# Kernel tuning notes

Measured on AMD Instinct MI355X. Metric: run time of the kernel, lower is better.

The kernel has to match this reference:

```python
import jax, jax.numpy as jnp
import numpy as np
from jax import lax

BIG = 1e10  # initial 'infinite' distance, matching torch's 1e10


def farthest_point_sample(xyz, npoint):
    # xyz: [B, N, 3] float; returns centroids: [B, npoint] int32
    B, N, _ = xyz.shape

    def step(carry, _):
        distance, farthest = carry            # [B,N], [B]
        # gather current farthest point per batch -> [B,1,3]
        centroid = jnp.take_along_axis(xyz, farthest[:, None, None], axis=1)
        dist = jnp.sum((xyz - centroid) ** 2, axis=-1)   # [B,N]
        distance = jnp.minimum(distance, dist)           # running min distance
        new_farthest = jnp.argmax(distance, axis=-1).astype(jnp.int32)
        # emit the index selected at THIS iteration (torch stores before update)
        return (distance, new_farthest), farthest

    init = (jnp.full((B, N), BIG, dtype=xyz.dtype),
            jnp.zeros((B,), dtype=jnp.int32))
    _, centroids = lax.scan(step, init, None, length=npoint)  # [npoint, B]
    return centroids.T  # [B, npoint]


def setup_inputs() -> dict:
    key = jax.random.key(0)
    B, N = 8, 131072
    xyz = jax.random.normal(key, (B, N, 3), dtype=jnp.float32)
    return {"xyz": xyz, "points": 1024}


def reference(xyz, points):
    return farthest_point_sample(xyz, points)
```

## Files before the change

kernel.cpp:

```cpp
#include <hip/hip_runtime.h>
#include <stdint.h>


#define NPTS        131072
#define NBATCH      8
#define WGB         32
#define THREADS     256
#define PPW         4096
#define SLOT_STRIDE 16
#define BIGDIST     1e10f

__global__ __launch_bounds__(THREADS, 1) void fps_kernel(
        const float* __restrict__ xyz,
        int* __restrict__ out,
        unsigned long long* __restrict__ slots,
        int npoint)
{
    const int bid  = blockIdx.x;
    const int b    = bid & (NBATCH - 1);
    const int w    = bid >> 3;
    const int tid  = threadIdx.x;
    const int lane = tid & 63;
    const int wave = tid >> 6;

    const float* base = xyz + (size_t)b * NPTS * 3;
    const int q0 = w * PPW;

    __shared__ __align__(16) float x_lds[PPW];
    __shared__ __align__(16) float y_lds[PPW];
    __shared__ __align__(16) float z_lds[PPW];
    __shared__ unsigned long long s_w[THREADS / 64];
    __shared__ float s_c[3];

    #pragma unroll
    for (int j = 0; j < 16; ++j) {
        int q = tid + 256 * j;
        const float* p = base + (size_t)(q0 + q) * 3;
        x_lds[q] = p[0];
        y_lds[q] = p[1];
        z_lds[q] = p[2];
    }

    float dist[16];
    #pragma unroll
    for (int j = 0; j < 16; ++j) dist[j] = BIGDIST;

    float cx = base[0], cy = base[1], cz = base[2];

    if (w == 0 && tid == 0) out[b * npoint + 0] = 0;

    const size_t PAR = (size_t)NBATCH * WGB * SLOT_STRIDE;

    __syncthreads();

    for (int i = 0; i < npoint - 1; ++i) {
        float bv = -1.0f; int bq = 0;
        {
            #pragma clang fp contract(off)
            #pragma unroll
            for (int g = 0; g < 4; ++g) {
                const int qg = 4 * tid + 1024 * g;
                float4 xv = *reinterpret_cast<const float4*>(&x_lds[qg]);
                float4 yv = *reinterpret_cast<const float4*>(&y_lds[qg]);
                float4 zv = *reinterpret_cast<const float4*>(&z_lds[qg]);
                float xs[4] = { xv.x, xv.y, xv.z, xv.w };
                float ys[4] = { yv.x, yv.y, yv.z, yv.w };
                float zs[4] = { zv.x, zv.y, zv.z, zv.w };
                #pragma unroll
                for (int e = 0; e < 4; ++e) {
                    const int j = 4 * g + e;
                    float dx = xs[e] - cx, dy = ys[e] - cy, dz = zs[e] - cz;
                    float d  = dx*dx + dy*dy + dz*dz;
                    float nd = fminf(dist[j], d);
                    dist[j]  = nd;
                    if (nd > bv) { bv = nd; bq = qg + e; }
                }
            }
        }
        unsigned long long pk =
              ((unsigned long long)__float_as_uint(bv) << 32)
            | (unsigned long long)(0x1FFFFu - (unsigned)(q0 + bq));

        #pragma unroll
        for (int m = 32; m >= 1; m >>= 1) {
            unsigned long long o = __shfl_xor(pk, m);
            if (o > pk) pk = o;
        }
        if (lane == 0) s_w[wave] = pk;
        __syncthreads();

        unsigned long long* sb =
            slots + ((i & 1) ? PAR : (size_t)0) + (size_t)b * WGB * SLOT_STRIDE;
        const unsigned tag = (unsigned)(i + 1);

        if (wave == 0) {
            unsigned long long v = s_w[lane & 3];
            #pragma unroll
            for (int m = 2; m >= 1; m >>= 1) {
                unsigned long long o = __shfl_xor(v, m);
                if (o > v) v = o;
            }
            if (lane == 0) {
                unsigned long long pub = v | ((unsigned long long)tag << 22);
                __hip_atomic_store(sb + (size_t)w * SLOT_STRIDE, pub,
                                   __ATOMIC_RELAXED, __HIP_MEMORY_SCOPE_AGENT);
            }
            unsigned long long s = 0;
            if (lane < WGB) {
                unsigned long long* sl = sb + (size_t)lane * SLOT_STRIDE;
                do {
                    s = __hip_atomic_load(sl, __ATOMIC_RELAXED,
                                          __HIP_MEMORY_SCOPE_AGENT);
                } while (((unsigned)(s >> 22) & 1023u) != tag);
            }
            int idx_l = (int)(0x1FFFFu - (unsigned)(s & 0x1FFFFu));
            float ccx = 0.f, ccy = 0.f, ccz = 0.f;
            if (lane < WGB) {
                const float* cp = base + (size_t)idx_l * 3;
                ccx = cp[0]; ccy = cp[1]; ccz = cp[2];
            }
            unsigned long long mx = s;
            #pragma unroll
            for (int m = 16; m >= 1; m >>= 1) {
                unsigned long long o = __shfl_xor(mx, m);
                if (o > mx) mx = o;
            }
            unsigned long long ball = __ballot(lane < WGB && s == mx);
            int winlane = __ffsll(ball) - 1;
            float wx = __shfl(ccx, winlane);
            float wy = __shfl(ccy, winlane);
            float wz = __shfl(ccz, winlane);
            int  wix = __shfl(idx_l, winlane);
            if (lane == 0) {
                s_c[0] = wx; s_c[1] = wy; s_c[2] = wz;
                if (w == 0) out[b * npoint + (i + 1)] = wix;
            }
        }
        __syncthreads();

        cx = s_c[0]; cy = s_c[1]; cz = s_c[2];
    }
}

extern "C" void kernel_launch(void* const* d_in, const int* in_sizes, int n_in,
                              void* d_out, int out_size, void* d_ws, size_t ws_size,
                              hipStream_t stream) {
    const float* xyz = (const float*)d_in[0];
    int* out = (int*)d_out;
    unsigned long long* slots = (unsigned long long*)d_ws;
    const int npoint = out_size / NBATCH;

    hipMemsetAsync(d_ws, 0,
                   (size_t)2 * NBATCH * WGB * SLOT_STRIDE * sizeof(unsigned long long),
                   stream);

    dim3 grid(NBATCH * WGB);
    dim3 block(THREADS);
    fps_kernel<<<grid, block, 0, stream>>>(xyz, out, slots, npoint);
}
```

Baseline: 2.345 ms.

## Publish per-wave results globally and drop intra-block barriers in FPS loop

Each wave now publishes its own argmax candidate to a global slot (128 slots per batch instead of 32), and every wave independently polls all slots and reduces them. This removes both __syncthreads and the LDS hand-off of the centroid from every iteration. Point coordinates are also cached in registers instead of being reloaded from LDS each iteration. The trade-off is four times more global polling traffic and redundant reductions in every wave, plus higher register pressure.

```diff
diff --git a/kernel.cpp b/kernel.cpp
--- a/kernel.cpp
+++ b/kernel.cpp
@@ -7,6 +7,7 @@
 #define WGB         32
 #define THREADS     256
 #define PPW         4096
+#define NSLOT       (WGB * 4)
 #define SLOT_STRIDE 16
 #define BIGDIST     1e10f
 
@@ -21,7 +22,7 @@
     const int w    = bid >> 3;
     const int tid  = threadIdx.x;
     const int lane = tid & 63;
-    const int wave = tid >> 6;
+    const int v    = tid >> 6;
 
     const float* base = xyz + (size_t)b * NPTS * 3;
     const int q0 = w * PPW;
@@ -29,8 +30,6 @@
     __shared__ __align__(16) float x_lds[PPW];
     __shared__ __align__(16) float y_lds[PPW];
     __shared__ __align__(16) float z_lds[PPW];
-    __shared__ unsigned long long s_w[THREADS / 64];
-    __shared__ float s_c[3];
 
     #pragma unroll
     for (int j = 0; j < 16; ++j) {
@@ -40,7 +39,17 @@
         y_lds[q] = p[1];
         z_lds[q] = p[2];
     }
+    __syncthreads();
 
+    const int pbase = q0 + 1024 * v + 4 * lane;
+    float4 X[4], Y[4], Z[4];
+    #pragma unroll
+    for (int g = 0; g < 4; ++g) {
+        const int qg = 1024 * v + 4 * lane + 256 * g;
+        X[g] = *reinterpret_cast<const float4*>(&x_lds[qg]);
+        Y[g] = *reinterpret_cast<const float4*>(&y_lds[qg]);
+        Z[g] = *reinterpret_cast<const float4*>(&z_lds[qg]);
+    }
     float dist[16];
     #pragma unroll
     for (int j = 0; j < 16; ++j) dist[j] = BIGDIST;
@@ -49,23 +58,19 @@
 
     if (w == 0 && tid == 0) out[b * npoint + 0] = 0;
 
-    const size_t PAR = (size_t)NBATCH * WGB * SLOT_STRIDE;
-
-    __syncthreads();
+    const size_t PAR = (size_t)NBATCH * NSLOT * SLOT_STRIDE;
+    unsigned long long* sbase = slots + (size_t)b * NSLOT * SLOT_STRIDE;
+    const int sid = (w << 2) | v;
 
     for (int i = 0; i < npoint - 1; ++i) {
-        float bv = -1.0f; int bq = 0;
+        float bv = -1.0f; int boff = 0;
         {
             #pragma clang fp contract(off)
             #pragma unroll
             for (int g = 0; g < 4; ++g) {
-                const int qg = 4 * tid + 1024 * g;
-                float4 xv = *reinterpret_cast<const float4*>(&x_lds[qg]);
-                float4 yv = *reinterpret_cast<const float4*>(&y_lds[qg]);
-                float4 zv = *reinterpret_cast<const float4*>(&z_lds[qg]);
-                float xs[4] = { xv.x, xv.y, xv.z, xv.w };
-                float ys[4] = { yv.x, yv.y, yv.z, yv.w };
-                float zs[4] = { zv.x, zv.y, zv.z, zv.w };
+                float xs[4] = { X[g].x, X[g].y, X[g].z, X[g].w };
+                float ys[4] = { Y[g].x, Y[g].y, Y[g].z, Y[g].w };
+                float zs[4] = { Z[g].x, Z[g].y, Z[g].z, Z[g].w };
                 #pragma unroll
                 for (int e = 0; e < 4; ++e) {
                     const int j = 4 * g + e;
@@ -73,72 +78,63 @@
                     float d  = dx*dx + dy*dy + dz*dz;
                     float nd = fminf(dist[j], d);
                     dist[j]  = nd;
-                    if (nd > bv) { bv = nd; bq = qg + e; }
+                    if (nd > bv) { bv = nd; boff = 256 * g + e; }
                 }
             }
         }
         unsigned long long pk =
               ((unsigned long long)__float_as_uint(bv) << 32)
-            | (unsigned long long)(0x1FFFFu - (unsigned)(q0 + bq));
+            | (unsigned long long)(0x1FFFFu - (unsigned)(pbase + boff));
 
         #pragma unroll
         for (int m = 32; m >= 1; m >>= 1) {
             unsigned long long o = __shfl_xor(pk, m);
             if (o > pk) pk = o;
         }
-        if (lane == 0) s_w[wave] = pk;
-        __syncthreads();
 
-        unsigned long long* sb =
-            slots + ((i & 1) ? PAR : (size_t)0) + (size_t)b * WGB * SLOT_STRIDE;
+        unsigned long long* sb = sbase + ((i & 1) ? PAR : (size_t)0);
         const unsigned tag = (unsigned)(i + 1);
 
-        if (wave == 0) {
-            unsigned long long v = s_w[lane & 3];
-            #pragma unroll
-            for (int m = 2; m >= 1; m >>= 1) {
-                unsigned long long o = __shfl_xor(v, m);
-                if (o > v) v = o;
+        if (lane == 0) {
+            __hip_atomic_store(sb + (size_t)sid * SLOT_STRIDE,
+                               pk | ((unsigned long long)tag << 22),
+                               __ATOMIC_RELAXED, __HIP_MEMORY_SCOPE_AGENT);
+        }
+
+        unsigned long long* a0 = sb + (size_t)(2 * lane)     * SLOT_STRIDE;
+        unsigned long long* a1 = sb + (size_t)(2 * lane + 1) * SLOT_STRIDE;
+        unsigned long long s0 = 0, s1 = 0;
+        bool ok0 = false, ok1 = false;
+        do {
+            if (!ok0) {
+                s0 = __hip_atomic_load(a0, __ATOMIC_RELAXED, __HIP_MEMORY_SCOPE_AGENT);
+                ok0 = ((unsigned)(s0 >> 22) & 1023u) == tag;
             }
-            if (lane == 0) {
-                unsigned long long pub = v | ((unsigned long long)tag << 22);
-                __hip_atomic_store(sb + (size_t)w * SLOT_STRIDE, pub,
-                                   __ATOMIC_RELAXED, __HIP_MEMORY_SCOPE_AGENT);
+            if (!ok1) {
+                s1 = __hip_atomic_load(a1, __ATOMIC_RELAXED, __HIP_MEMORY_SCOPE_AGENT);
+                ok1 = ((unsigned)(s1 >> 22) & 1023u) == tag;
             }
-            unsigned long long s = 0;
-            if (lane < WGB) {
-                unsigned long long* sl = sb + (size_t)lane * SLOT_STRIDE;
-                do {
-                    s = __hip_atomic_load(sl, __ATOMIC_RELAXED,
-                                          __HIP_MEMORY_SCOPE_AGENT);
-                } while (((unsigned)(s >> 22) & 1023u) != tag);
-            }
-            int idx_l = (int)(0x1FFFFu - (unsigned)(s & 0x1FFFFu));
-            float ccx = 0.f, ccy = 0.f, ccz = 0.f;
-            if (lane < WGB) {
-                const float* cp = base + (size_t)idx_l * 3;
-                ccx = cp[0]; ccy = cp[1]; ccz = cp[2];
-            }
-            unsigned long long mx = s;
-            #pragma unroll
-            for (int m = 16; m >= 1; m >>= 1) {
-                unsigned long long o = __shfl_xor(mx, m);
-                if (o > mx) mx = o;
-            }
-            unsigned long long ball = __ballot(lane < WGB && s == mx);
-            int winlane = __ffsll(ball) - 1;
-            float wx = __shfl(ccx, winlane);
-            float wy = __shfl(ccy, winlane);
-            float wz = __shfl(ccz, winlane);
-            int  wix = __shfl(idx_l, winlane);
-            if (lane == 0) {
-                s_c[0] = wx; s_c[1] = wy; s_c[2] = wz;
-                if (w == 0) out[b * npoint + (i + 1)] = wix;
-            }
+        } while (!(ok0 && ok1));
+
+        unsigned long long m2 = (s0 > s1) ? s0 : s1;
+        int idx_l = (int)(0x1FFFFu - (unsigned)(m2 & 0x1FFFFu));
+        const float* cp = base + (size_t)idx_l * 3;
+        float ccx = cp[0], ccy = cp[1], ccz = cp[2];
+
+        unsigned long long mx = m2;
+        #pragma unroll
+        for (int m = 32; m >= 1; m >>= 1) {
+            unsigned long long o = __shfl_xor(mx, m);
+            if (o > mx) mx = o;
         }
-        __syncthreads();
+        unsigned long long ball = __ballot(m2 == mx);
+        int winlane = __ffsll(ball) - 1;
+        cx = __shfl(ccx, winlane);
+        cy = __shfl(ccy, winlane);
+        cz = __shfl(ccz, winlane);
+        int wix = __shfl(idx_l, winlane);
 
-        cx = s_c[0]; cy = s_c[1]; cz = s_c[2];
+        if (w == 0 && tid == 0) out[b * npoint + (i + 1)] = wix;
     }
 }
 
@@ -151,7 +147,7 @@
     const int npoint = out_size / NBATCH;
 
     hipMemsetAsync(d_ws, 0,
-                   (size_t)2 * NBATCH * WGB * SLOT_STRIDE * sizeof(unsigned long long),
+                   (size_t)2 * NBATCH * NSLOT * SLOT_STRIDE * sizeof(unsigned long long),
                    stream);
 
     dim3 grid(NBATCH * WGB);
```

Result: slower. 3.059 ms (+30.4%).

## Publish winner coordinates in slots and keep point coords in registers

Applied to the files above, without the earlier changes.

Each workgroup now publishes its local winner's x/y/z (tagged) alongside the packed distance/index in its global slot. The waiting wave then reads all 32 slots with two lanes per slot, so the dependent global gather of the winning point's coordinates after the spin-wait disappears from the critical path. Each thread's 16 points are also loaded once from LDS into registers pinned with empty asm, and the points per thread are now contiguous, removing per-iteration LDS reads. The cost is more atomic stores and polling loads per iteration and higher register pressure; relaxed ordering across the four stores relies on per-word tags.

```diff
diff --git a/kernel.cpp b/kernel.cpp
--- a/kernel.cpp
+++ b/kernel.cpp
@@ -7,13 +7,19 @@
 #define WGB         32
 #define THREADS     256
 #define PPW         4096
+#define PPL         16
 #define SLOT_STRIDE 16
 #define BIGDIST     1e10f
+
+typedef unsigned long long u64;
+
+#define LIST16(M) M(0) M(1) M(2) M(3) M(4) M(5) M(6) M(7) \
+                  M(8) M(9) M(10) M(11) M(12) M(13) M(14) M(15)
 
 __global__ __launch_bounds__(THREADS, 1) void fps_kernel(
         const float* __restrict__ xyz,
         int* __restrict__ out,
-        unsigned long long* __restrict__ slots,
+        u64* __restrict__ slots,
         int npoint)
 {
     const int bid  = blockIdx.x;
@@ -21,7 +27,7 @@
     const int w    = bid >> 3;
     const int tid  = threadIdx.x;
     const int lane = tid & 63;
-    const int wave = tid >> 6;
+    const int v    = tid >> 6;
 
     const float* base = xyz + (size_t)b * NPTS * 3;
     const int q0 = w * PPW;
@@ -29,8 +35,9 @@
     __shared__ __align__(16) float x_lds[PPW];
     __shared__ __align__(16) float y_lds[PPW];
     __shared__ __align__(16) float z_lds[PPW];
-    __shared__ unsigned long long s_w[THREADS / 64];
+    __shared__ u64   s_w[THREADS / 64];
     __shared__ float s_c[3];
+    __shared__ int   s_f;
 
     #pragma unroll
     for (int j = 0; j < 16; ++j) {
@@ -40,105 +47,111 @@
         y_lds[q] = p[1];
         z_lds[q] = p[2];
     }
+    __syncthreads();
 
-    float dist[16];
-    #pragma unroll
-    for (int j = 0; j < 16; ++j) dist[j] = BIGDIST;
+    const int qb    = tid * PPL;
+    const int pbase = q0 + qb;
+
+    #define DECLC(j) float x##j = x_lds[qb + j], y##j = y_lds[qb + j], z##j = z_lds[qb + j];
+    LIST16(DECLC)
+    #define PINC(j) asm volatile("" : "+v"(x##j), "+v"(y##j), "+v"(z##j));
+    LIST16(PINC)
+    #define DECLD(j) float d##j = BIGDIST;
+    LIST16(DECLD)
 
     float cx = base[0], cy = base[1], cz = base[2];
-
     if (w == 0 && tid == 0) out[b * npoint + 0] = 0;
 
     const size_t PAR = (size_t)NBATCH * WGB * SLOT_STRIDE;
-
-    __syncthreads();
+    u64* sbase = slots + (size_t)b * WGB * SLOT_STRIDE;
 
     for (int i = 0; i < npoint - 1; ++i) {
-        float bv = -1.0f; int bq = 0;
+        float bv = -1.0f; int bj = 0;
         {
             #pragma clang fp contract(off)
-            #pragma unroll
-            for (int g = 0; g < 4; ++g) {
-                const int qg = 4 * tid + 1024 * g;
-                float4 xv = *reinterpret_cast<const float4*>(&x_lds[qg]);
-                float4 yv = *reinterpret_cast<const float4*>(&y_lds[qg]);
-                float4 zv = *reinterpret_cast<const float4*>(&z_lds[qg]);
-                float xs[4] = { xv.x, xv.y, xv.z, xv.w };
-                float ys[4] = { yv.x, yv.y, yv.z, yv.w };
-                float zs[4] = { zv.x, zv.y, zv.z, zv.w };
-                #pragma unroll
-                for (int e = 0; e < 4; ++e) {
-                    const int j = 4 * g + e;
-                    float dx = xs[e] - cx, dy = ys[e] - cy, dz = zs[e] - cz;
-                    float d  = dx*dx + dy*dy + dz*dz;
-                    float nd = fminf(dist[j], d);
-                    dist[j]  = nd;
-                    if (nd > bv) { bv = nd; bq = qg + e; }
-                }
-            }
+            #define UPD(j) { float dx = x##j - cx, dy = y##j - cy, dz = z##j - cz; \
+                             float dd = dx*dx + dy*dy + dz*dz;   \
+                             float nd = fminf(d##j, dd); d##j = nd;                  \
+                             if (nd > bv) { bv = nd; bj = j; } }
+            LIST16(UPD)
         }
-        unsigned long long pk =
-              ((unsigned long long)__float_as_uint(bv) << 32)
-            | (unsigned long long)(0x1FFFFu - (unsigned)(q0 + bq));
+        u64 pk = ((u64)__float_as_uint(bv) << 32)
+               | (u64)(0x1FFFFu - (unsigned)(pbase + bj));
 
         #pragma unroll
         for (int m = 32; m >= 1; m >>= 1) {
-            unsigned long long o = __shfl_xor(pk, m);
+            u64 o = __shfl_xor(pk, m);
             if (o > pk) pk = o;
         }
-        if (lane == 0) s_w[wave] = pk;
+        if (lane == 0) s_w[v] = pk;
         __syncthreads();
 
-        unsigned long long* sb =
-            slots + ((i & 1) ? PAR : (size_t)0) + (size_t)b * WGB * SLOT_STRIDE;
+        u64* sb = sbase + ((i & 1) ? PAR : (size_t)0);
         const unsigned tag = (unsigned)(i + 1);
 
-        if (wave == 0) {
-            unsigned long long v = s_w[lane & 3];
-            #pragma unroll
-            for (int m = 2; m >= 1; m >>= 1) {
-                unsigned long long o = __shfl_xor(v, m);
-                if (o > v) v = o;
-            }
+        if (v == 0) {
+            u64 c = s_w[lane & 3];
+            u64 o1 = __shfl_xor(c, 1); if (o1 > c) c = o1;
+            u64 o2 = __shfl_xor(c, 2); if (o2 > c) c = o2;
+
             if (lane == 0) {
-                unsigned long long pub = v | ((unsigned long long)tag << 22);
-                __hip_atomic_store(sb + (size_t)w * SLOT_STRIDE, pub,
+                int idx_wg = (int)(0x1FFFFu - (unsigned)(c & 0x1FFFFu));
+                int qw = idx_wg - q0;
+                u64 tw = ((u64)tag << 32);
+                u64* my = sb + (size_t)w * SLOT_STRIDE;
+                __hip_atomic_store(my + 1, tw | (u64)__float_as_uint(x_lds[qw]),
+                                   __ATOMIC_RELAXED, __HIP_MEMORY_SCOPE_AGENT);
+                __hip_atomic_store(my + 2, tw | (u64)__float_as_uint(y_lds[qw]),
+                                   __ATOMIC_RELAXED, __HIP_MEMORY_SCOPE_AGENT);
+                __hip_atomic_store(my + 3, tw | (u64)__float_as_uint(z_lds[qw]),
+                                   __ATOMIC_RELAXED, __HIP_MEMORY_SCOPE_AGENT);
+                __hip_atomic_store(my + 0, c | ((u64)tag << 22),
                                    __ATOMIC_RELAXED, __HIP_MEMORY_SCOPE_AGENT);
             }
-            unsigned long long s = 0;
-            if (lane < WGB) {
-                unsigned long long* sl = sb + (size_t)lane * SLOT_STRIDE;
-                do {
-                    s = __hip_atomic_load(sl, __ATOMIC_RELAXED,
-                                          __HIP_MEMORY_SCOPE_AGENT);
-                } while (((unsigned)(s >> 22) & 1023u) != tag);
-            }
-            int idx_l = (int)(0x1FFFFu - (unsigned)(s & 0x1FFFFu));
-            float ccx = 0.f, ccy = 0.f, ccz = 0.f;
-            if (lane < WGB) {
-                const float* cp = base + (size_t)idx_l * 3;
-                ccx = cp[0]; ccy = cp[1]; ccz = cp[2];
-            }
-            unsigned long long mx = s;
+
+            const int  s    = lane >> 1;
+            const bool even = (lane & 1) == 0;
+            u64* sp = sb + (size_t)s * SLOT_STRIDE + (even ? 0 : 2);
+            u64 wa = 0, wb = 0;
+            bool oka = false, okb = false;
+            do {
+                if (!oka) {
+                    wa = __hip_atomic_load(sp + 0, __ATOMIC_RELAXED,
+                                           __HIP_MEMORY_SCOPE_AGENT);
+                    unsigned t = even ? (unsigned)((wa >> 22) & 1023u)
+                                      : (unsigned)((wa >> 32) & 1023u);
+                    oka = (t == tag);
+                }
+                if (!okb) {
+                    wb = __hip_atomic_load(sp + 1, __ATOMIC_RELAXED,
+                                           __HIP_MEMORY_SCOPE_AGENT);
+                    okb = ((unsigned)((wb >> 32) & 1023u) == tag);
+                }
+            } while (__ballot(oka && okb) != ~0ULL);
+
+            u64 mx = even ? wa : 0;
             #pragma unroll
-            for (int m = 16; m >= 1; m >>= 1) {
-                unsigned long long o = __shfl_xor(mx, m);
+            for (int m = 32; m >= 1; m >>= 1) {
+                u64 o = __shfl_xor(mx, m);
                 if (o > mx) mx = o;
             }
-            unsigned long long ball = __ballot(lane < WGB && s == mx);
-            int winlane = __ffsll(ball) - 1;
-            float wx = __shfl(ccx, winlane);
-            float wy = __shfl(ccy, winlane);
-            float wz = __shfl(ccz, winlane);
-            int  wix = __shfl(idx_l, winlane);
+            int idx_win = (int)(0x1FFFFu - (unsigned)(mx & 0x1FFFFu));
+            int sw = idx_win >> 12;
+
+            float fx = even ? __uint_as_float((unsigned)wb) : 0.f;
+            float fy = even ? 0.f : __uint_as_float((unsigned)wa);
+            float fz = even ? 0.f : __uint_as_float((unsigned)wb);
+            float nx = __shfl(fx, 2 * sw);
+            float ny = __shfl(fy, 2 * sw + 1);
+            float nz = __shfl(fz, 2 * sw + 1);
             if (lane == 0) {
-                s_c[0] = wx; s_c[1] = wy; s_c[2] = wz;
-                if (w == 0) out[b * npoint + (i + 1)] = wix;
+                s_c[0] = nx; s_c[1] = ny; s_c[2] = nz; s_f = idx_win;
             }
         }
         __syncthreads();
 
         cx = s_c[0]; cy = s_c[1]; cz = s_c[2];
+        if (w == 0 && tid == 0) out[b * npoint + (i + 1)] = s_f;
     }
 }
 
@@ -147,11 +160,11 @@
                               hipStream_t stream) {
     const float* xyz = (const float*)d_in[0];
     int* out = (int*)d_out;
-    unsigned long long* slots = (unsigned long long*)d_ws;
+    u64* slots = (u64*)d_ws;
     const int npoint = out_size / NBATCH;
 
     hipMemsetAsync(d_ws, 0,
-                   (size_t)2 * NBATCH * WGB * SLOT_STRIDE * sizeof(unsigned long long),
+                   (size_t)2 * NBATCH * WGB * SLOT_STRIDE * sizeof(u64),
                    stream);
 
     dim3 grid(NBATCH * WGB);
```

Result: slower. 2.893 ms (+23.3%).

## Detect same-XCD batch groups and use workgroup-scope atomics for slot exchange

Applied to the files above, without the earlier changes.

Adds a startup census in which each workgroup publishes its XCC id. If all 32 workgroups of a batch sit on the same XCD, the per-iteration slot publish and poll use atomic exchange and fetch_or at workgroup scope instead of agent-scope store and load, aiming to keep the cross-workgroup reduction in the local L2 and cut sync latency. The fallback path is unchanged. Because block ids interleave batches (b = bid & 7), the XCD placement decides whether the fast path is ever taken, and the correctness of workgroup-scope atomics across CUs relies on hardware behaviour.

```diff
diff --git a/kernel.cpp b/kernel.cpp
--- a/kernel.cpp
+++ b/kernel.cpp
@@ -10,10 +10,12 @@
 #define SLOT_STRIDE 16
 #define BIGDIST     1e10f
 
+typedef unsigned long long u64;
+
 __global__ __launch_bounds__(THREADS, 1) void fps_kernel(
         const float* __restrict__ xyz,
         int* __restrict__ out,
-        unsigned long long* __restrict__ slots,
+        u64* __restrict__ ws,
         int npoint)
 {
     const int bid  = blockIdx.x;
@@ -21,7 +23,7 @@
     const int w    = bid >> 3;
     const int tid  = threadIdx.x;
     const int lane = tid & 63;
-    const int wave = tid >> 6;
+    const int v    = tid >> 6;
 
     const float* base = xyz + (size_t)b * NPTS * 3;
     const int q0 = w * PPW;
@@ -29,8 +31,10 @@
     __shared__ __align__(16) float x_lds[PPW];
     __shared__ __align__(16) float y_lds[PPW];
     __shared__ __align__(16) float z_lds[PPW];
-    __shared__ unsigned long long s_w[THREADS / 64];
+    __shared__ u64   s_w[THREADS / 64];
     __shared__ float s_c[3];
+    __shared__ int   s_f;
+    __shared__ int   s_fast;
 
     #pragma unroll
     for (int j = 0; j < 16; ++j) {
@@ -41,17 +45,44 @@
         z_lds[q] = p[2];
     }
 
+    u64* slots  = ws;
+    u64* census = ws + (size_t)2 * NBATCH * WGB * SLOT_STRIDE;
+
+    if (v == 0) {
+        unsigned xcc;
+        asm volatile("s_getreg_b32 %0, hwreg(HW_REG_XCC_ID)" : "=s"(xcc));
+        u64* cb = census + (size_t)b * WGB * SLOT_STRIDE;
+        if (lane == 0) {
+            __hip_atomic_store(cb + (size_t)w * SLOT_STRIDE,
+                               (0xC0DEC0DEull << 32) | (u64)xcc,
+                               __ATOMIC_RELAXED, __HIP_MEMORY_SCOPE_AGENT);
+        }
+        u64 cv = 0;
+        if (lane < WGB) {
+            u64* cl = cb + (size_t)lane * SLOT_STRIDE;
+            do {
+                cv = __hip_atomic_load(cl, __ATOMIC_RELAXED,
+                                       __HIP_MEMORY_SCOPE_AGENT);
+            } while ((cv >> 32) != 0xC0DEC0DEull);
+        }
+        unsigned my = (unsigned)cv;
+        unsigned x0 = __shfl(my, 0);
+        bool same = (lane >= WGB) || (my == x0);
+        if (lane == 0) s_fast = (__ballot(same) == ~0ull) ? 1 : 0;
+    }
+
     float dist[16];
     #pragma unroll
     for (int j = 0; j < 16; ++j) dist[j] = BIGDIST;
 
     float cx = base[0], cy = base[1], cz = base[2];
-
     if (w == 0 && tid == 0) out[b * npoint + 0] = 0;
 
+    __syncthreads();
+    const int fast = s_fast;
+
     const size_t PAR = (size_t)NBATCH * WGB * SLOT_STRIDE;
-
-    __syncthreads();
+    u64* sbase = slots + (size_t)b * WGB * SLOT_STRIDE;
 
     for (int i = 0; i < npoint - 1; ++i) {
         float bv = -1.0f; int bq = 0;
@@ -77,41 +108,51 @@
                 }
             }
         }
-        unsigned long long pk =
-              ((unsigned long long)__float_as_uint(bv) << 32)
-            | (unsigned long long)(0x1FFFFu - (unsigned)(q0 + bq));
+        u64 pk = ((u64)__float_as_uint(bv) << 32)
+               | (u64)(0x1FFFFu - (unsigned)(q0 + bq));
 
         #pragma unroll
         for (int m = 32; m >= 1; m >>= 1) {
-            unsigned long long o = __shfl_xor(pk, m);
+            u64 o = __shfl_xor(pk, m);
             if (o > pk) pk = o;
         }
-        if (lane == 0) s_w[wave] = pk;
+        if (lane == 0) s_w[v] = pk;
         __syncthreads();
 
-        unsigned long long* sb =
-            slots + ((i & 1) ? PAR : (size_t)0) + (size_t)b * WGB * SLOT_STRIDE;
+        u64* sb = sbase + ((i & 1) ? PAR : (size_t)0);
         const unsigned tag = (unsigned)(i + 1);
 
-        if (wave == 0) {
-            unsigned long long v = s_w[lane & 3];
-            #pragma unroll
-            for (int m = 2; m >= 1; m >>= 1) {
-                unsigned long long o = __shfl_xor(v, m);
-                if (o > v) v = o;
-            }
+        if (v == 0) {
+            u64 c = s_w[lane & 3];
+            u64 o1 = __shfl_xor(c, 1); if (o1 > c) c = o1;
+            u64 o2 = __shfl_xor(c, 2); if (o2 > c) c = o2;
+
             if (lane == 0) {
-                unsigned long long pub = v | ((unsigned long long)tag << 22);
-                __hip_atomic_store(sb + (size_t)w * SLOT_STRIDE, pub,
-                                   __ATOMIC_RELAXED, __HIP_MEMORY_SCOPE_AGENT);
-            }
-            unsigned long long s = 0;
+                u64 pub = c | ((u64)tag << 22);
+                u64* my = sb + (size_t)w * SLOT_STRIDE;
+                if (fast) {
+                    __hip_atomic_exchange(my, pub, __ATOMIC_RELAXED,
+                                          __HIP_MEMORY_SCOPE_WORKGROUP);
+                } else {
+                    __hip_atomic_store(my, pub, __ATOMIC_RELAXED,
+                                       __HIP_MEMORY_SCOPE_AGENT);
+                }
+            }
+
+            u64 s = 0;
             if (lane < WGB) {
-                unsigned long long* sl = sb + (size_t)lane * SLOT_STRIDE;
-                do {
-                    s = __hip_atomic_load(sl, __ATOMIC_RELAXED,
-                                          __HIP_MEMORY_SCOPE_AGENT);
-                } while (((unsigned)(s >> 22) & 1023u) != tag);
+                u64* sl = sb + (size_t)lane * SLOT_STRIDE;
+                if (fast) {
+                    do {
+                        s = __hip_atomic_fetch_or(sl, 0ull, __ATOMIC_RELAXED,
+                                                  __HIP_MEMORY_SCOPE_WORKGROUP);
+                    } while (((unsigned)(s >> 22) & 1023u) != tag);
+                } else {
+                    do {
+                        s = __hip_atomic_load(sl, __ATOMIC_RELAXED,
+                                              __HIP_MEMORY_SCOPE_AGENT);
+                    } while (((unsigned)(s >> 22) & 1023u) != tag);
+                }
             }
             int idx_l = (int)(0x1FFFFu - (unsigned)(s & 0x1FFFFu));
             float ccx = 0.f, ccy = 0.f, ccz = 0.f;
@@ -119,20 +160,20 @@
                 const float* cp = base + (size_t)idx_l * 3;
                 ccx = cp[0]; ccy = cp[1]; ccz = cp[2];
             }
-            unsigned long long mx = s;
+            u64 mx = s;
             #pragma unroll
-            for (int m = 16; m >= 1; m >>= 1) {
-                unsigned long long o = __shfl_xor(mx, m);
+            for (int m = 32; m >= 1; m >>= 1) {
+                u64 o = __shfl_xor(mx, m);
                 if (o > mx) mx = o;
             }
-            unsigned long long ball = __ballot(lane < WGB && s == mx);
+            u64 ball = __ballot(lane < WGB && s == mx);
             int winlane = __ffsll(ball) - 1;
             float wx = __shfl(ccx, winlane);
             float wy = __shfl(ccy, winlane);
             float wz = __shfl(ccz, winlane);
             int  wix = __shfl(idx_l, winlane);
             if (lane == 0) {
-                s_c[0] = wx; s_c[1] = wy; s_c[2] = wz;
+                s_c[0] = wx; s_c[1] = wy; s_c[2] = wz; s_f = wix;
                 if (w == 0) out[b * npoint + (i + 1)] = wix;
             }
         }
@@ -147,14 +188,14 @@
                               hipStream_t stream) {
     const float* xyz = (const float*)d_in[0];
     int* out = (int*)d_out;
-    unsigned long long* slots = (unsigned long long*)d_ws;
+    u64* ws = (u64*)d_ws;
     const int npoint = out_size / NBATCH;
 
     hipMemsetAsync(d_ws, 0,
-                   (size_t)2 * NBATCH * WGB * SLOT_STRIDE * sizeof(unsigned long long),
+                   (size_t)(2 * NBATCH * WGB + NBATCH * WGB) * SLOT_STRIDE * sizeof(u64),
                    stream);
 
     dim3 grid(NBATCH * WGB);
     dim3 block(THREADS);
-    fps_kernel<<<grid, block, 0, stream>>>(xyz, out, slots, npoint);
+    fps_kernel<<<grid, block, 0, stream>>>(xyz, out, ws, npoint);
 }
```

Measured after the change: 2.384 ms. No clear change (+1.6%).
